# Kernel optimization log

Hardware: AMD Instinct MI355X
Metric: run time of the kernel (lower is better)

## Reference

```python
import jax, jax.numpy as jnp
import numpy as np

N_NODES = 50000
N_EDGES = 640000
N_GRAPHS = 64
IN_DIM, HID, OUT_DIM = 128, 256, 4


def gcn_conv(x, src, dst, W, b, n_nodes):
    """PyG GCNConv: linear transform, then sym-normalized aggregation with self-loops."""
    h = x @ W  # [N, out]
    deg = jnp.zeros((n_nodes,), h.dtype).at[dst].add(1.0) + 1.0  # +1 self-loop
    dinv = jax.lax.rsqrt(deg)  # deg >= 1 always
    norm = dinv[src] * dinv[dst]  # [E]
    msg = h[src] * norm[:, None]  # [E, out]  gather + scale
    agg = jax.ops.segment_sum(msg, dst, num_segments=n_nodes)  # scatter-add
    agg = agg + h * (dinv * dinv)[:, None]  # self-loop contribution
    return agg + b


def global_mean_pool(x, batch, num_graphs):
    s = jax.ops.segment_sum(x, batch, num_segments=num_graphs)
    cnt = jax.ops.segment_sum(jnp.ones((x.shape[0],), x.dtype), batch, num_segments=num_graphs)
    return s / jnp.clip(cnt, 1.0)[:, None]


def setup_inputs() -> dict:
    key = jax.random.key(0)
    ks = jax.random.split(key, 8)
    x = jax.random.normal(ks[0], (N_NODES, IN_DIM), jnp.float32)
    src = jax.random.randint(ks[1], (N_EDGES,), 0, N_NODES, jnp.int64 if jax.config.jax_enable_x64 else jnp.int32)
    dst = jax.random.randint(ks[2], (N_EDGES,), 0, N_NODES, src.dtype)
    batch = jnp.sort(jax.random.randint(ks[3], (N_NODES,), 0, N_GRAPHS, src.dtype))
    W1 = jax.random.normal(ks[4], (IN_DIM, HID), jnp.float32) * (1.0 / np.sqrt(IN_DIM))
    b1 = jnp.zeros((HID,), jnp.float32)
    W2 = jax.random.normal(ks[5], (HID, HID // 2), jnp.float32) * (1.0 / np.sqrt(HID))
    b2 = jnp.zeros((HID // 2,), jnp.float32)
    Wfc = jax.random.normal(ks[6], (HID // 2, OUT_DIM), jnp.float32) * (1.0 / np.sqrt(HID // 2))
    bfc = jnp.zeros((OUT_DIM,), jnp.float32)
    return {"x": x, "src": src, "dst": dst, "batch": batch,
            "W1": W1, "b1": b1, "W2": W2, "b2": b2, "Wfc": Wfc, "bfc": bfc}


def reference(x, src, dst, batch, W1, b1, W2, b2, Wfc, bfc):
    n = x.shape[0]
    h = jax.nn.relu(gcn_conv(x, src, dst, W1, b1, n))   # dropout is identity at inference
    h = jax.nn.relu(gcn_conv(h, src, dst, W2, b2, n))
    g = global_mean_pool(h, batch, N_GRAPHS)            # [G, HID//2]
    return g @ Wfc + bfc                                # [G, OUT_DIM]
```

## Files before the change

### kernel.cpp

```cpp
#include <hip/hip_runtime.h>


constexpr int IN_DIM  = 128;
constexpr int HID     = 256;
constexpr int HID2    = 128;
constexpr int OUT_DIM = 4;
constexpr int NGRAPH  = 64;
constexpr int PCH     = 64;
constexpr int TP      = 132;

typedef __attribute__((ext_vector_type(8))) short bf16x8;
typedef __attribute__((ext_vector_type(4))) float f32x4;

__device__ __forceinline__ short f2bf(float f) {
    union { float f; unsigned u; } v; v.f = f;
    unsigned r = v.u + 0x7fff + ((v.u >> 16) & 1);
    return (short)(r >> 16);
}
__device__ __forceinline__ float bf2f(short s) {
    union { unsigned u; float f; } v; v.u = ((unsigned)(unsigned short)s) << 16;
    return v.f;
}


__global__ void wprep_all_kernel(const float* __restrict__ W1, short* __restrict__ W1th,
                                 short* __restrict__ W1tl,
                                 const float* __restrict__ W2, short* __restrict__ W2th,
                                 short* __restrict__ W2tl,
                                 int* __restrict__ count, int N) {
    int i = blockIdx.x * blockDim.x + threadIdx.x;
    if (i < IN_DIM * HID) {
        int k = i / HID, n = i % HID;
        float w = W1[i];
        short h = f2bf(w);
        W1th[n * IN_DIM + k] = h;
        W1tl[n * IN_DIM + k] = f2bf(w - bf2f(h));
    }
    if (i < HID * HID2) {
        int k = i / HID2, n = i % HID2;
        float w = W2[i];
        short h = f2bf(w);
        W2th[n * HID + k] = h;
        W2tl[n * HID + k] = f2bf(w - bf2f(h));
    }
    if (i < N) count[i] = 0;
}


__global__ void hist_kernel(const int* __restrict__ dst, int* __restrict__ count,
                            ushort* __restrict__ rank, int E) {
    int i = blockIdx.x * blockDim.x + threadIdx.x;
    if (i < E) rank[i] = (ushort)atomicAdd(&count[dst[i]], 1);
}

__global__ void scan1_kernel(const int* __restrict__ count, int* __restrict__ bsums, int N) {
    __shared__ int s[256];
    int t = threadIdx.x, i = blockIdx.x * 256 + t;
    int v = (i < N) ? count[i] : 0;
    s[t] = v; __syncthreads();
    for (int o = 1; o < 256; o <<= 1) {
        int x = (t >= o) ? s[t - o] : 0;
        __syncthreads(); s[t] += x; __syncthreads();
    }
    if (t == 255) bsums[blockIdx.x] = s[255];
}

__global__ void scan2_kernel(int* __restrict__ bsums, int nb, float* __restrict__ pool) {
    __shared__ int s[256];
    int t = threadIdx.x;
    int v = (t < nb) ? bsums[t] : 0;
    s[t] = v; __syncthreads();
    for (int o = 1; o < 256; o <<= 1) {
        int x = (t >= o) ? s[t - o] : 0;
        __syncthreads(); s[t] += x; __syncthreads();
    }
    if (t < nb) bsums[t] = s[t] - v;
    for (int i = t; i < NGRAPH * HID2; i += 256) pool[i] = 0.f;
}

__global__ void scan3_kernel(const int* __restrict__ count, const int* __restrict__ bsums,
                             int* __restrict__ rowptr, float* __restrict__ dinv, int N, int E) {
    __shared__ int s[256];
    int t = threadIdx.x, i = blockIdx.x * 256 + t;
    int v = (i < N) ? count[i] : 0;
    s[t] = v; __syncthreads();
    for (int o = 1; o < 256; o <<= 1) {
        int x = (t >= o) ? s[t - o] : 0;
        __syncthreads(); s[t] += x; __syncthreads();
    }
    if (i < N) {
        int ex = bsums[blockIdx.x] + s[t] - v;
        rowptr[i] = ex;
        dinv[i] = rsqrtf((float)v + 1.0f);
        if (i == 0) rowptr[N] = E;
    }
}

__global__ void scatter_scale_kernel(const int* __restrict__ src, const int* __restrict__ dst,
                                     const ushort* __restrict__ rank,
                                     const int* __restrict__ rowptr, ushort* __restrict__ csr,
                                     const float* __restrict__ x, const float* __restrict__ dinv,
                                     ushort* __restrict__ xb, int E, int total2) {
    int i = blockIdx.x * blockDim.x + threadIdx.x;
    if (i < E) {
        int p = rowptr[dst[i]] + (int)rank[i];
        csr[p] = (ushort)src[i];
    }
    if (i < total2) {
        float d = dinv[i >> 6];
        float2 v = ((const float2*)x)[i];
        ushort2 o;
        o.x = (ushort)f2bf(v.x * d);
        o.y = (ushort)f2bf(v.y * d);
        ((ushort2*)xb)[i] = o;
    }
}


template <int K, int N, bool ALO, bool RELU, bool SCALED>
__launch_bounds__(256)
__global__ void gemm_tile_kernel(const short* __restrict__ Ah, const short* __restrict__ Al,
                                 const short* __restrict__ Bh, const short* __restrict__ Bl,
                                 const float* __restrict__ bias,
                                 const float* __restrict__ dinv,
                                 short* __restrict__ Cb, int M) {
    __shared__ __align__(16) short LDSBUF[128 * TP];
    short (*S)[8][512] = (short (*)[8][512])LDSBUF;

    const int tid  = threadIdx.x;
    const int wave = tid >> 6;
    const int lane = tid & 63;
    const int row0 = blockIdx.y * 128;
    const int col0 = blockIdx.x * 128;

    const int l15 = lane & 15;
    const int kq  = (lane >> 4) * 8;

    f32x4 acc[4][4];
#pragma unroll
    for (int i = 0; i < 4; ++i)
#pragma unroll
        for (int j = 0; j < 4; ++j) acc[i][j] = f32x4{0.f, 0.f, 0.f, 0.f};

    const int mt0 = (wave & 1) * 4;
    const int nt0 = (wave >> 1) * 4;

    for (int kb = 0; kb < K; kb += 32) {
        if (ALO) {
            const short* gsrc = (wave == 0) ? Ah : (wave == 1) ? Al : (wave == 2) ? Bh : Bl;
            const bool isA = wave < 2;
            const int rb = (isA ? row0 : col0) + l15;
            bf16x8 stg[8];
#pragma unroll
            for (int j = 0; j < 8; ++j) {
                int rr = rb + j * 16;
                if (isA && rr >= M) rr = M - 1;
                stg[j] = *(const bf16x8*)(gsrc + (size_t)rr * K + kb + kq);
            }
#pragma unroll
            for (int j = 0; j < 8; ++j)
                *(bf16x8*)&S[wave][j][lane * 8] = stg[j];
        } else {
            if (wave < 2) {
                const int rb = row0 + l15;
                bf16x8 stg[4];
#pragma unroll
                for (int j = 0; j < 4; ++j) {
                    int rr = rb + (wave * 4 + j) * 16;
                    if (rr >= M) rr = M - 1;
                    stg[j] = *(const bf16x8*)(Ah + (size_t)rr * K + kb + kq);
                }
#pragma unroll
                for (int j = 0; j < 4; ++j)
                    *(bf16x8*)&S[0][wave * 4 + j][lane * 8] = stg[j];
            } else {
                const short* gsrc = (wave == 2) ? Bh : Bl;
                const int rb = col0 + l15;
                bf16x8 stg[8];
#pragma unroll
                for (int j = 0; j < 8; ++j)
                    stg[j] = *(const bf16x8*)(gsrc + (size_t)(rb + j * 16) * K + kb + kq);
#pragma unroll
                for (int j = 0; j < 8; ++j)
                    *(bf16x8*)&S[wave][j][lane * 8] = stg[j];
            }
        }
        __syncthreads();

        bf16x8 ah[4], al[4], bh[4], bl[4];
#pragma unroll
        for (int i = 0; i < 4; ++i) {
            ah[i] = *(const bf16x8*)&S[0][mt0 + i][lane * 8];
            if (ALO) al[i] = *(const bf16x8*)&S[1][mt0 + i][lane * 8];
            bh[i] = *(const bf16x8*)&S[2][nt0 + i][lane * 8];
            bl[i] = *(const bf16x8*)&S[3][nt0 + i][lane * 8];
        }
#pragma unroll
        for (int i = 0; i < 4; ++i)
#pragma unroll
            for (int j = 0; j < 4; ++j) {
                acc[i][j] = __builtin_amdgcn_mfma_f32_16x16x32_bf16(ah[i], bh[j], acc[i][j], 0, 0, 0);
                acc[i][j] = __builtin_amdgcn_mfma_f32_16x16x32_bf16(ah[i], bl[j], acc[i][j], 0, 0, 0);
                if (ALO)
                    acc[i][j] = __builtin_amdgcn_mfma_f32_16x16x32_bf16(al[i], bh[j], acc[i][j], 0, 0, 0);
            }
        __syncthreads();
    }

    short* T = LDSBUF;
    const int lrow_b = (wave & 1) * 64 + (lane >> 4) * 4;
    const int lcol_b = (wave >> 1) * 64 + l15;
#pragma unroll
    for (int j = 0; j < 4; ++j) {
        int lcol = lcol_b + j * 16;
        float bv = RELU ? bias[col0 + lcol] : 0.f;
#pragma unroll
        for (int i = 0; i < 4; ++i) {
#pragma unroll
            for (int r = 0; r < 4; ++r) {
                int lrow = lrow_b + i * 16 + r;
                float v = acc[i][j][r];
                if (RELU) v = fmaxf(v + bv, 0.f);
                if (SCALED) {
                    int dr = row0 + lrow; if (dr >= M) dr = M - 1;
                    v *= dinv[dr];
                }
                T[lrow * TP + lcol] = f2bf(v);
            }
        }
    }
    __syncthreads();
#pragma unroll
    for (int it = 0; it < 8; ++it) {
        int chunk = it * 256 + tid;
        int lr = chunk >> 4;
        int lc = (chunk & 15) * 8;
        int grow = row0 + lr;
        if (grow < M)
            *(bf16x8*)(Cb + (size_t)grow * N + col0 + lc) = *(const bf16x8*)&T[lr * TP + lc];
    }
}


template <bool BR>
__launch_bounds__(256)
__global__ void agg_gather_kernel(const ushort* __restrict__ hb, const float* __restrict__ dinv,
                                  const int* __restrict__ rowptr, const ushort* __restrict__ csr,
                                  const float* __restrict__ bias,
                                  short* __restrict__ oh, int N) {
    int wid = (blockIdx.x * blockDim.x + threadIdx.x) >> 6;
    int lane = threadIdx.x & 63;
    if (wid >= N) return;
    int lo = rowptr[wid], hi = rowptr[wid + 1];
    float dd = dinv[wid];

    unsigned sv = *(const unsigned*)(hb + ((size_t)wid << 7) + (lane << 1));
    float a0x = bf2f((short)(sv & 0xffff)), a0y = bf2f((short)(sv >> 16));
    float a1x = 0.f, a1y = 0.f, a2x = 0.f, a2y = 0.f, a3x = 0.f, a3y = 0.f;
    float a4x = 0.f, a4y = 0.f, a5x = 0.f, a5y = 0.f, a6x = 0.f, a6y = 0.f;
    float a7x = 0.f, a7y = 0.f;

    const ushort* hptr = hb + (lane << 1);

    for (int base = lo; base < hi; base += 64) {
        int cnt = min(64, hi - base);
        int sidx = (int)csr[base + (lane < cnt ? lane : cnt - 1)];
        int j = 0;
        for (; j + 8 <= cnt; j += 8) {
            int s0 = __shfl(sidx, j + 0, 64);
            int s1 = __shfl(sidx, j + 1, 64);
            int s2 = __shfl(sidx, j + 2, 64);
            int s3 = __shfl(sidx, j + 3, 64);
            int s4 = __shfl(sidx, j + 4, 64);
            int s5 = __shfl(sidx, j + 5, 64);
            int s6 = __shfl(sidx, j + 6, 64);
            int s7 = __shfl(sidx, j + 7, 64);
            unsigned p0 = *(const unsigned*)(hptr + ((size_t)s0 << 7));
            unsigned p1 = *(const unsigned*)(hptr + ((size_t)s1 << 7));
            unsigned p2 = *(const unsigned*)(hptr + ((size_t)s2 << 7));
            unsigned p3 = *(const unsigned*)(hptr + ((size_t)s3 << 7));
            unsigned p4 = *(const unsigned*)(hptr + ((size_t)s4 << 7));
            unsigned p5 = *(const unsigned*)(hptr + ((size_t)s5 << 7));
            unsigned p6 = *(const unsigned*)(hptr + ((size_t)s6 << 7));
            unsigned p7 = *(const unsigned*)(hptr + ((size_t)s7 << 7));
            a0x += bf2f((short)(p0 & 0xffff)); a0y += bf2f((short)(p0 >> 16));
            a1x += bf2f((short)(p1 & 0xffff)); a1y += bf2f((short)(p1 >> 16));
            a2x += bf2f((short)(p2 & 0xffff)); a2y += bf2f((short)(p2 >> 16));
            a3x += bf2f((short)(p3 & 0xffff)); a3y += bf2f((short)(p3 >> 16));
            a4x += bf2f((short)(p4 & 0xffff)); a4y += bf2f((short)(p4 >> 16));
            a5x += bf2f((short)(p5 & 0xffff)); a5y += bf2f((short)(p5 >> 16));
            a6x += bf2f((short)(p6 & 0xffff)); a6y += bf2f((short)(p6 >> 16));
            a7x += bf2f((short)(p7 & 0xffff)); a7y += bf2f((short)(p7 >> 16));
        }
        for (; j + 4 <= cnt; j += 4) {
            int s0 = __shfl(sidx, j + 0, 64);
            int s1 = __shfl(sidx, j + 1, 64);
            int s2 = __shfl(sidx, j + 2, 64);
            int s3 = __shfl(sidx, j + 3, 64);
            unsigned p0 = *(const unsigned*)(hptr + ((size_t)s0 << 7));
            unsigned p1 = *(const unsigned*)(hptr + ((size_t)s1 << 7));
            unsigned p2 = *(const unsigned*)(hptr + ((size_t)s2 << 7));
            unsigned p3 = *(const unsigned*)(hptr + ((size_t)s3 << 7));
            a0x += bf2f((short)(p0 & 0xffff)); a0y += bf2f((short)(p0 >> 16));
            a1x += bf2f((short)(p1 & 0xffff)); a1y += bf2f((short)(p1 >> 16));
            a2x += bf2f((short)(p2 & 0xffff)); a2y += bf2f((short)(p2 >> 16));
            a3x += bf2f((short)(p3 & 0xffff)); a3y += bf2f((short)(p3 >> 16));
        }
        for (; j < cnt; ++j) {
            int s = __shfl(sidx, j, 64);
            unsigned pv = *(const unsigned*)(hptr + ((size_t)s << 7));
            a0x += bf2f((short)(pv & 0xffff)); a0y += bf2f((short)(pv >> 16));
        }
    }

    float rx = dd * (((a0x + a1x) + (a2x + a3x)) + ((a4x + a5x) + (a6x + a7x)));
    float ry = dd * (((a0y + a1y) + (a2y + a3y)) + ((a4y + a5y) + (a6y + a7y)));
    if (BR) {
        float2 b = ((const float2*)bias)[lane];
        rx = fmaxf(rx + b.x, 0.f);
        ry = fmaxf(ry + b.y, 0.f);
    }
    short2 hv; hv.x = f2bf(rx); hv.y = f2bf(ry);
    *(short2*)&oh[(size_t)wid * 128 + lane * 2] = hv;
}


__launch_bounds__(128)
__global__ void pool_kernel(const ushort* __restrict__ h, const int* __restrict__ batch,
                            float* __restrict__ pool, int N) {
    int c = threadIdx.x;
    int i0 = blockIdx.x * PCH;
    if (i0 >= N) return;
    int i1 = min(i0 + PCH, N);
    int g = batch[i0];
    float acc = 0.f;
#pragma unroll 4
    for (int i = i0; i < i1; ++i) {
        int gi = batch[i];
        if (gi != g) {
            atomicAdd(&pool[g * HID2 + c], acc);
            acc = 0.f; g = gi;
        }
        acc += bf2f((short)h[(size_t)i * HID2 + c]);
    }
    atomicAdd(&pool[g * HID2 + c], acc);
}

__device__ __forceinline__ int lower_bound_i(const int* __restrict__ a, int n, int key) {
    int lo = 0, hi = n;
    while (lo < hi) {
        int mid = (lo + hi) >> 1;
        if (a[mid] < key) lo = mid + 1; else hi = mid;
    }
    return lo;
}

__global__ void fc_kernel(const float* __restrict__ pool, const int* __restrict__ batch,
                          const float* __restrict__ Wfc, const float* __restrict__ bfc,
                          float* __restrict__ out, int N) {
    int t = threadIdx.x;
    int g = t >> 2, o = t & 3;
    int lo = lower_bound_i(batch, N, g);
    int hi = lower_bound_i(batch, N, g + 1);
    float acc = 0.f;
#pragma unroll 8
    for (int c = 0; c < HID2; ++c)
        acc = fmaf(pool[g * HID2 + c], Wfc[c * OUT_DIM + o], acc);
    float inv = 1.0f / fmaxf((float)(hi - lo), 1.0f);
    out[g * OUT_DIM + o] = acc * inv + bfc[o];
}

extern "C" void kernel_launch(void* const* d_in, const int* in_sizes, int n_in,
                              void* d_out, int out_size, void* d_ws, size_t ws_size,
                              hipStream_t stream) {
    const float* x   = (const float*)d_in[0];
    const int* src   = (const int*)d_in[1];
    const int* dst   = (const int*)d_in[2];
    const int* batch = (const int*)d_in[3];
    const float* W1  = (const float*)d_in[4];
    const float* b1  = (const float*)d_in[5];
    const float* W2  = (const float*)d_in[6];
    const float* b2  = (const float*)d_in[7];
    const float* Wfc = (const float*)d_in[8];
    const float* bfc = (const float*)d_in[9];
    float* out = (float*)d_out;

    const int N = in_sizes[0] / IN_DIM;
    const int E = in_sizes[1];
    const int NB = (N + 255) / 256;

    char* ws = (char*)d_ws;
    size_t off = 0;
    auto alloc = [&](size_t bytes) {
        char* p = ws + off;
        off = (off + bytes + 255) & ~(size_t)255;
        return p;
    };
    float*  dinv   = (float*) alloc((size_t)N * 4);
    int*    count  = (int*)   alloc((size_t)N * 4);
    int*    rowptr = (int*)   alloc((size_t)(N + 1) * 4);
    int*    bsums  = (int*)   alloc(256 * 4);
    ushort* rank   = (ushort*)alloc((size_t)E * 2);
    ushort* csr    = (ushort*)alloc((size_t)E * 2);
    short*  W1th   = (short*) alloc((size_t)IN_DIM * HID * 2);
    short*  W1tl   = (short*) alloc((size_t)IN_DIM * HID * 2);
    short*  W2th   = (short*) alloc((size_t)HID * HID2 * 2);
    short*  W2tl   = (short*) alloc((size_t)HID * HID2 * 2);
    ushort* xb     = (ushort*)alloc((size_t)N * IN_DIM * 2);
    short*  axb    = (short*) alloc((size_t)N * IN_DIM * 2);
    short*  a1h    = (short*) alloc((size_t)N * HID * 2);
    float*  pool   = (float*) alloc((size_t)NGRAPH * HID2 * 4);
    ushort* h2b = xb;
    short*  a2b = axb;

    wprep_all_kernel<<<(max(IN_DIM * HID, N) + 255) / 256, 256, 0, stream>>>(
        W1, W1th, W1tl, W2, W2th, W2tl, count, N);

    hist_kernel<<<(E + 255) / 256, 256, 0, stream>>>(dst, count, rank, E);
    scan1_kernel<<<NB, 256, 0, stream>>>(count, bsums, N);
    scan2_kernel<<<1, 256, 0, stream>>>(bsums, NB, pool);
    scan3_kernel<<<NB, 256, 0, stream>>>(count, bsums, rowptr, dinv, N, E);
    scatter_scale_kernel<<<(N * 64 + 255) / 256, 256, 0, stream>>>(
        src, dst, rank, rowptr, csr, x, dinv, xb, E, N * 64);

    agg_gather_kernel<false><<<(N + 3) / 4, 256, 0, stream>>>(
        xb, dinv, rowptr, csr, nullptr, axb, N);
    gemm_tile_kernel<IN_DIM, HID, false, true, false>
        <<<dim3(HID / 128, (N + 127) / 128), 256, 0, stream>>>(
        axb, nullptr, W1th, W1tl, b1, nullptr, a1h, N);

    gemm_tile_kernel<HID, HID2, false, false, true>
        <<<dim3(HID2 / 128, (N + 127) / 128), 256, 0, stream>>>(
        a1h, nullptr, W2th, W2tl, nullptr, dinv, (short*)h2b, N);
    agg_gather_kernel<true><<<(N + 3) / 4, 256, 0, stream>>>(
        h2b, dinv, rowptr, csr, b2, a2b, N);

    pool_kernel<<<(N + PCH - 1) / PCH, HID2, 0, stream>>>((const ushort*)a2b, batch, pool, N);
    fc_kernel<<<1, NGRAPH * OUT_DIM, 0, stream>>>(pool, batch, Wfc, bfc, out, N);
}
```

Before: 259.7 us.

## Gather neighbor rows with 16-byte loads, four edges per wavefront pass

Restructures the CSR aggregation kernel so each 16-lane quarter-wave loads a full 128-element bf16 row with 16-byte vector loads. The four quarters handle four different edges at once, and partial sums are combined with xor-shuffles at the end. This replaces per-lane 4-byte loads with wider, fewer memory instructions and puts more independent rows in flight. The cost is the cross-lane reduction and masked tail handling, and only a quarter of the lanes write the output.

```diff
diff --git a/kernel.cpp b/kernel.cpp
--- a/kernel.cpp
+++ b/kernel.cpp
@@ -254,74 +254,84 @@
     int lo = rowptr[wid], hi = rowptr[wid + 1];
     float dd = dinv[wid];
 
-    unsigned sv = *(const unsigned*)(hb + ((size_t)wid << 7) + (lane << 1));
-    float a0x = bf2f((short)(sv & 0xffff)), a0y = bf2f((short)(sv >> 16));
-    float a1x = 0.f, a1y = 0.f, a2x = 0.f, a2y = 0.f, a3x = 0.f, a3y = 0.f;
-    float a4x = 0.f, a4y = 0.f, a5x = 0.f, a5y = 0.f, a6x = 0.f, a6y = 0.f;
-    float a7x = 0.f, a7y = 0.f;
-
-    const ushort* hptr = hb + (lane << 1);
+    const int g  = lane >> 4;
+    const int li = lane & 15;
+
+    float a[8];
+    {
+        bf16x8 sv = *(const bf16x8*)(hb + ((size_t)wid << 7) + (li << 3));
+#pragma unroll
+        for (int d = 0; d < 8; ++d) a[d] = (g == 0) ? bf2f(sv[d]) : 0.f;
+    }
+
+    const ushort* hrow = hb + (li << 3);
 
     for (int base = lo; base < hi; base += 64) {
         int cnt = min(64, hi - base);
         int sidx = (int)csr[base + (lane < cnt ? lane : cnt - 1)];
         int j = 0;
-        for (; j + 8 <= cnt; j += 8) {
-            int s0 = __shfl(sidx, j + 0, 64);
-            int s1 = __shfl(sidx, j + 1, 64);
-            int s2 = __shfl(sidx, j + 2, 64);
-            int s3 = __shfl(sidx, j + 3, 64);
-            int s4 = __shfl(sidx, j + 4, 64);
-            int s5 = __shfl(sidx, j + 5, 64);
-            int s6 = __shfl(sidx, j + 6, 64);
-            int s7 = __shfl(sidx, j + 7, 64);
-            unsigned p0 = *(const unsigned*)(hptr + ((size_t)s0 << 7));
-            unsigned p1 = *(const unsigned*)(hptr + ((size_t)s1 << 7));
-            unsigned p2 = *(const unsigned*)(hptr + ((size_t)s2 << 7));
-            unsigned p3 = *(const unsigned*)(hptr + ((size_t)s3 << 7));
-            unsigned p4 = *(const unsigned*)(hptr + ((size_t)s4 << 7));
-            unsigned p5 = *(const unsigned*)(hptr + ((size_t)s5 << 7));
-            unsigned p6 = *(const unsigned*)(hptr + ((size_t)s6 << 7));
-            unsigned p7 = *(const unsigned*)(hptr + ((size_t)s7 << 7));
-            a0x += bf2f((short)(p0 & 0xffff)); a0y += bf2f((short)(p0 >> 16));
-            a1x += bf2f((short)(p1 & 0xffff)); a1y += bf2f((short)(p1 >> 16));
-            a2x += bf2f((short)(p2 & 0xffff)); a2y += bf2f((short)(p2 >> 16));
-            a3x += bf2f((short)(p3 & 0xffff)); a3y += bf2f((short)(p3 >> 16));
-            a4x += bf2f((short)(p4 & 0xffff)); a4y += bf2f((short)(p4 >> 16));
-            a5x += bf2f((short)(p5 & 0xffff)); a5y += bf2f((short)(p5 >> 16));
-            a6x += bf2f((short)(p6 & 0xffff)); a6y += bf2f((short)(p6 >> 16));
-            a7x += bf2f((short)(p7 & 0xffff)); a7y += bf2f((short)(p7 >> 16));
-        }
-        for (; j + 4 <= cnt; j += 4) {
-            int s0 = __shfl(sidx, j + 0, 64);
-            int s1 = __shfl(sidx, j + 1, 64);
-            int s2 = __shfl(sidx, j + 2, 64);
-            int s3 = __shfl(sidx, j + 3, 64);
-            unsigned p0 = *(const unsigned*)(hptr + ((size_t)s0 << 7));
-            unsigned p1 = *(const unsigned*)(hptr + ((size_t)s1 << 7));
-            unsigned p2 = *(const unsigned*)(hptr + ((size_t)s2 << 7));
-            unsigned p3 = *(const unsigned*)(hptr + ((size_t)s3 << 7));
-            a0x += bf2f((short)(p0 & 0xffff)); a0y += bf2f((short)(p0 >> 16));
-            a1x += bf2f((short)(p1 & 0xffff)); a1y += bf2f((short)(p1 >> 16));
-            a2x += bf2f((short)(p2 & 0xffff)); a2y += bf2f((short)(p2 >> 16));
-            a3x += bf2f((short)(p3 & 0xffff)); a3y += bf2f((short)(p3 >> 16));
-        }
-        for (; j < cnt; ++j) {
-            int s = __shfl(sidx, j, 64);
-            unsigned pv = *(const unsigned*)(hptr + ((size_t)s << 7));
-            a0x += bf2f((short)(pv & 0xffff)); a0y += bf2f((short)(pv >> 16));
-        }
-    }
-
-    float rx = dd * (((a0x + a1x) + (a2x + a3x)) + ((a4x + a5x) + (a6x + a7x)));
-    float ry = dd * (((a0y + a1y) + (a2y + a3y)) + ((a4y + a5y) + (a6y + a7y)));
+        for (; j + 32 <= cnt; j += 32) {
+            bf16x8 p[8];
+#pragma unroll
+            for (int u = 0; u < 8; ++u) {
+                int s = __shfl(sidx, j + u * 4 + g, 64);
+                p[u] = *(const bf16x8*)(hrow + ((size_t)s << 7));
+            }
+#pragma unroll
+            for (int u = 0; u < 8; ++u)
+#pragma unroll
+                for (int d = 0; d < 8; ++d) a[d] += bf2f(p[u][d]);
+        }
+        for (; j + 16 <= cnt; j += 16) {
+            bf16x8 p[4];
+#pragma unroll
+            for (int u = 0; u < 4; ++u) {
+                int s = __shfl(sidx, j + u * 4 + g, 64);
+                p[u] = *(const bf16x8*)(hrow + ((size_t)s << 7));
+            }
+#pragma unroll
+            for (int u = 0; u < 4; ++u)
+#pragma unroll
+                for (int d = 0; d < 8; ++d) a[d] += bf2f(p[u][d]);
+        }
+        if (j < cnt) {
+            bf16x8 p[4];
+            int e[4];
+#pragma unroll
+            for (int u = 0; u < 4; ++u) {
+                e[u] = j + u * 4 + g;
+                int s = __shfl(sidx, e[u] < cnt ? e[u] : cnt - 1, 64);
+                p[u] = *(const bf16x8*)(hrow + ((size_t)s << 7));
+            }
+#pragma unroll
+            for (int u = 0; u < 4; ++u) {
+                bool v = e[u] < cnt;
+#pragma unroll
+                for (int d = 0; d < 8; ++d) a[d] += v ? bf2f(p[u][d]) : 0.f;
+            }
+        }
+    }
+
+#pragma unroll
+    for (int d = 0; d < 8; ++d) {
+        a[d] += __shfl_xor(a[d], 16, 64);
+        a[d] += __shfl_xor(a[d], 32, 64);
+        a[d] *= dd;
+    }
     if (BR) {
-        float2 b = ((const float2*)bias)[lane];
-        rx = fmaxf(rx + b.x, 0.f);
-        ry = fmaxf(ry + b.y, 0.f);
-    }
-    short2 hv; hv.x = f2bf(rx); hv.y = f2bf(ry);
-    *(short2*)&oh[(size_t)wid * 128 + lane * 2] = hv;
+        float4 b0 = ((const float4*)bias)[li * 2];
+        float4 b1 = ((const float4*)bias)[li * 2 + 1];
+        a[0] = fmaxf(a[0] + b0.x, 0.f); a[1] = fmaxf(a[1] + b0.y, 0.f);
+        a[2] = fmaxf(a[2] + b0.z, 0.f); a[3] = fmaxf(a[3] + b0.w, 0.f);
+        a[4] = fmaxf(a[4] + b1.x, 0.f); a[5] = fmaxf(a[5] + b1.y, 0.f);
+        a[6] = fmaxf(a[6] + b1.z, 0.f); a[7] = fmaxf(a[7] + b1.w, 0.f);
+    }
+    if (g == 0) {
+        bf16x8 o;
+#pragma unroll
+        for (int d = 0; d < 8; ++d) o[d] = f2bf(a[d]);
+        *(bf16x8*)&oh[(size_t)wid * 128 + li * 8] = o;
+    }
 }
 
 
```

Result: no change. 257.6 us (-0.8%).
